# Kernel optimization log

Hardware: AMD Instinct MI355X
Metric: run time of the kernel (lower is better)

## Reference

```python
import jax, jax.numpy as jnp
import numpy as np

SM_SCALE = 0.08838834764831845  # 1/sqrt(128)
Q_LEN, K_LEN, H, M, D = 1024, 1024, 8, 8, 128


def setup_inputs() -> dict:
    key = jax.random.key(0)
    k1, k2, k3, k4 = jax.random.split(key, 4)
    Q = jax.random.normal(k1, (Q_LEN, H, M, D), dtype=jnp.float32)
    K_expanded = jax.random.normal(k2, (K_LEN, H, M, D), dtype=jnp.float32)
    mask = jax.random.normal(k3, (Q_LEN, K_LEN), dtype=jnp.float32)
    sinks = jax.random.normal(k4, (H, M, Q_LEN, 1), dtype=jnp.float32)
    return {"Q": Q, "K_expanded": K_expanded, "mask": mask, "sinks": sinks}


def reference(Q, K_expanded, mask, sinks):
    # [h, m, q, k] scaled scores + additive mask
    QK = jnp.einsum('qhmd,khmd->hmqk', Q, K_expanded) * SM_SCALE
    QK = QK + mask[None, None, :, :]
    # append sink logits on the key axis -> [h, m, q, k+1]
    return jnp.concatenate([QK, sinks], axis=-1)
```

## Files before the change

kernel.cpp:

```cpp
#include <hip/hip_runtime.h>
#include <hip/hip_bf16.h>

#define QL 1024
#define KL 1024
#define HM 64
#define DD 128
#define SM_SCALE 0.08838834764831845f

#define BM 128
#define BN 128
#define LDPAD 136

typedef __bf16 bf16x8 __attribute__((ext_vector_type(8)));
typedef __bf16 bf16x4 __attribute__((ext_vector_type(4)));
typedef float floatx4 __attribute__((ext_vector_type(4)));

__global__ __launch_bounds__(256, 2)
void qk_kernel(const float* __restrict__ Qg, const float* __restrict__ Kg,
               const float* __restrict__ mask, float* __restrict__ out)
{
    const int g    = blockIdx.y;
    const int tile = blockIdx.x;
    const int qt = (tile >> 3) * BM;
    const int kt = (tile & 7) * BN;

    __shared__ __bf16 As[BM][LDPAD];
    __shared__ __bf16 Bs[BN][LDPAD];

    const int t = threadIdx.x;

    const float* Ag = Qg + (size_t)qt * (HM * DD) + (size_t)g * DD;
    const float* Bg = Kg + (size_t)kt * (HM * DD) + (size_t)g * DD;
#pragma unroll
    for (int j = 0; j < 16; ++j) {
        int c = t + 256 * j;
        int row = c >> 5;
        int c4  = c & 31;
        float4 a = *(const float4*)(Ag + (size_t)row * (HM * DD) + c4 * 4);
        float4 b = *(const float4*)(Bg + (size_t)row * (HM * DD) + c4 * 4);
        bf16x4 av = { (__bf16)a.x, (__bf16)a.y, (__bf16)a.z, (__bf16)a.w };
        bf16x4 bv = { (__bf16)b.x, (__bf16)b.y, (__bf16)b.z, (__bf16)b.w };
        *(bf16x4*)&As[row][c4 * 4] = av;
        *(bf16x4*)&Bs[row][c4 * 4] = bv;
    }
    __syncthreads();

    const int wave = t >> 6;
    const int lane = t & 63;
    const int wm = (wave & 1) * 64;
    const int wn = (wave >> 1) * 64;
    const int lr = lane & 15;
    const int quad = lane >> 4;

    floatx4 acc[4][4] = {};

#pragma unroll
    for (int ks = 0; ks < 4; ++ks) {
        const int d0 = ks * 32 + quad * 8;
        bf16x8 af[4], bf[4];
#pragma unroll
        for (int mi = 0; mi < 4; ++mi)
            af[mi] = *(const bf16x8*)&As[wm + mi * 16 + lr][d0];
#pragma unroll
        for (int ni = 0; ni < 4; ++ni)
            bf[ni] = *(const bf16x8*)&Bs[wn + ni * 16 + lr][d0];
#pragma unroll
        for (int mi = 0; mi < 4; ++mi)
#pragma unroll
            for (int ni = 0; ni < 4; ++ni)
                acc[mi][ni] = __builtin_amdgcn_mfma_f32_16x16x32_bf16(
                    af[mi], bf[ni], acc[mi][ni], 0, 0, 0);
    }

    const size_t obase = (size_t)g * QL * 1025;
#pragma unroll
    for (int mi = 0; mi < 4; ++mi) {
#pragma unroll
        for (int r = 0; r < 4; ++r) {
            int q = qt + wm + mi * 16 + quad * 4 + r;
            const float* mrow = mask + (size_t)q * KL;
            float* orow = out + obase + (size_t)q * 1025;
#pragma unroll
            for (int ni = 0; ni < 4; ++ni) {
                int k = kt + wn + ni * 16 + lr;
                orow[k] = acc[mi][ni][r] * SM_SCALE + mrow[k];
            }
        }
    }
}

__global__ void sink_kernel(const float* __restrict__ sinks, float* __restrict__ out)
{
    int idx = blockIdx.x * 256 + threadIdx.x;
    out[(size_t)idx * 1025 + 1024] = sinks[idx];
}

extern "C" void kernel_launch(void* const* d_in, const int* in_sizes, int n_in,
                              void* d_out, int out_size, void* d_ws, size_t ws_size,
                              hipStream_t stream)
{
    const float* Q     = (const float*)d_in[0];
    const float* K     = (const float*)d_in[1];
    const float* mask  = (const float*)d_in[2];
    const float* sinks = (const float*)d_in[3];
    float* out = (float*)d_out;

    sink_kernel<<<(HM * QL) / 256, 256, 0, stream>>>(sinks, out);
    qk_kernel<<<dim3(64, 64), 256, 0, stream>>>(Q, K, mask, out);
}
```

Baseline: 410.3 us.

## Pre-convert Q/K to bf16 workspace and stream K tiles with async LDS loads

Adds a conversion kernel that writes Q and K as head-contiguous bf16 into the workspace. The original kernel re-read fp32 Q and K for every 128x128 tile. A new main kernel keeps one Q tile's fragments in registers and loops over all 8 K tiles per block. Each K tile is fetched with global_load_lds async copies into an XOR-swizzled LDS buffer, overlapping the next tile's fetch with the current MFMA and output stores. Sink writes are folded into the same kernel, which adds an extra launch and workspace traffic but cuts redundant fp32 reads. The grid shrinks to 512 blocks, which may reduce occupancy on a large GPU.

```diff
diff --git a/kernel.cpp b/kernel.cpp
--- a/kernel.cpp
+++ b/kernel.cpp
@@ -7,13 +7,147 @@
 #define DD 128
 #define SM_SCALE 0.08838834764831845f
 
+typedef __bf16 bf16x8_t __attribute__((ext_vector_type(8)));
+typedef __bf16 bf16x4_t __attribute__((ext_vector_type(4)));
+typedef float floatx4_t __attribute__((ext_vector_type(4)));
+
+__device__ __forceinline__ void async_cp16(const void* g, void* l) {
+    __builtin_amdgcn_global_load_lds(
+        (const __attribute__((address_space(1))) void*)g,
+        (__attribute__((address_space(3))) void*)l, 16, 0, 0);
+}
+
+__global__ __launch_bounds__(256)
+void cvt_kernel(const float* __restrict__ Q, const float* __restrict__ K,
+                __bf16* __restrict__ Qb, __bf16* __restrict__ Kb)
+{
+    const int g = blockIdx.y, rc = blockIdx.x, t = threadIdx.x;
+    const size_t inb  = (size_t)(rc * 128) * (HM * DD) + (size_t)g * DD;
+    const size_t outb = (size_t)g * (QL * DD) + (size_t)(rc * 128) * DD;
+#pragma unroll
+    for (int j = 0; j < 16; ++j) {
+        int c = t + 256 * j, row = c >> 5, c4 = c & 31;
+        size_t go = inb + (size_t)row * (HM * DD) + c4 * 4;
+        size_t wo = outb + (size_t)row * DD + c4 * 4;
+        float4 a = *(const float4*)(Q + go);
+        float4 b = *(const float4*)(K + go);
+        bf16x4_t av = { (__bf16)a.x, (__bf16)a.y, (__bf16)a.z, (__bf16)a.w };
+        bf16x4_t bv = { (__bf16)b.x, (__bf16)b.y, (__bf16)b.z, (__bf16)b.w };
+        *(bf16x4_t*)(Qb + wo) = av;
+        *(bf16x4_t*)(Kb + wo) = bv;
+    }
+}
+
+__global__ __launch_bounds__(256, 2)
+void qk2_kernel(const __bf16* __restrict__ Qb, const __bf16* __restrict__ Kb,
+                const float* __restrict__ mask, const float* __restrict__ sinks,
+                float* __restrict__ out)
+{
+    const int g  = blockIdx.y;
+    const int qt = blockIdx.x * 128;
+
+    __shared__ __bf16 As[128 * DD];
+    __shared__ __bf16 Bs[128 * DD];
+
+    const int t = threadIdx.x, wave = t >> 6, lane = t & 63;
+    const int lr = lane & 15, quad = lane >> 4;
+    const int wm = (wave & 1) * 64, wn = (wave >> 1) * 64;
+
+    const __bf16* Atile  = Qb + (size_t)g * QL * DD + (size_t)qt * DD;
+    const __bf16* Ktile0 = Kb + (size_t)g * KL * DD;
+
+#pragma unroll
+    for (int i = 0; i < 8; ++i) {
+        int r = wave * 32 + i * 4 + (lane >> 4);
+        int s = lane & 15;
+        int c = s ^ (r & 15);
+        async_cp16(Atile + (size_t)r * DD + c * 8, As + (wave * 32 + i * 4) * DD);
+    }
+#pragma unroll
+    for (int i = 0; i < 8; ++i) {
+        int r = wave * 32 + i * 4 + (lane >> 4);
+        int s = lane & 15;
+        int c = s ^ (r & 15);
+        async_cp16(Ktile0 + (size_t)r * DD + c * 8, Bs + (wave * 32 + i * 4) * DD);
+    }
+    asm volatile("s_waitcnt vmcnt(0)" ::: "memory");
+    __syncthreads();
+
+    bf16x8_t af[4][4];
+#pragma unroll
+    for (int ks = 0; ks < 4; ++ks)
+#pragma unroll
+        for (int mi = 0; mi < 4; ++mi) {
+            int r = wm + mi * 16 + lr;
+            int c = ks * 4 + quad;
+            af[ks][mi] = *(const bf16x8_t*)&As[r * DD + (c ^ lr) * 8];
+        }
+
+    const size_t outg = (size_t)g * QL * 1025;
+
+#pragma unroll 1
+    for (int kt = 0; kt < 8; ++kt) {
+        bf16x8_t bfr[4][4];
+#pragma unroll
+        for (int ks = 0; ks < 4; ++ks)
+#pragma unroll
+            for (int ni = 0; ni < 4; ++ni) {
+                int r = wn + ni * 16 + lr;
+                int c = ks * 4 + quad;
+                bfr[ks][ni] = *(const bf16x8_t*)&Bs[r * DD + (c ^ lr) * 8];
+            }
+        __syncthreads();
+
+        if (kt < 7) {
+            const __bf16* Kt = Ktile0 + (size_t)(kt + 1) * 128 * DD;
+#pragma unroll
+            for (int i = 0; i < 8; ++i) {
+                int r = wave * 32 + i * 4 + (lane >> 4);
+                int s = lane & 15;
+                int c = s ^ (r & 15);
+                async_cp16(Kt + (size_t)r * DD + c * 8, Bs + (wave * 32 + i * 4) * DD);
+            }
+        }
+
+        floatx4_t acc[4][4] = {};
+#pragma unroll
+        for (int ks = 0; ks < 4; ++ks)
+#pragma unroll
+            for (int mi = 0; mi < 4; ++mi)
+#pragma unroll
+                for (int ni = 0; ni < 4; ++ni)
+                    acc[mi][ni] = __builtin_amdgcn_mfma_f32_16x16x32_bf16(
+                        af[ks][mi], bfr[ks][ni], acc[mi][ni], 0, 0, 0);
+
+#pragma unroll
+        for (int mi = 0; mi < 4; ++mi)
+#pragma unroll
+            for (int r4 = 0; r4 < 4; ++r4) {
+                int q = qt + wm + mi * 16 + quad * 4 + r4;
+                const float* mrow = mask + (size_t)q * KL + kt * 128;
+                float* orow = out + outg + (size_t)q * 1025 + kt * 128;
+#pragma unroll
+                for (int ni = 0; ni < 4; ++ni) {
+                    int k = wn + ni * 16 + lr;
+                    orow[k] = acc[mi][ni][r4] * SM_SCALE + mrow[k];
+                }
+            }
+
+        if (kt < 7) {
+            asm volatile("s_waitcnt vmcnt(0)" ::: "memory");
+            __syncthreads();
+        }
+    }
+
+    if (t < 128) {
+        int q = qt + t;
+        out[outg + (size_t)q * 1025 + 1024] = sinks[(size_t)g * QL + q];
+    }
+}
+
 #define BM 128
 #define BN 128
 #define LDPAD 136
-
-typedef __bf16 bf16x8 __attribute__((ext_vector_type(8)));
-typedef __bf16 bf16x4 __attribute__((ext_vector_type(4)));
-typedef float floatx4 __attribute__((ext_vector_type(4)));
 
 __global__ __launch_bounds__(256, 2)
 void qk_kernel(const float* __restrict__ Qg, const float* __restrict__ Kg,
@@ -38,10 +172,10 @@
         int c4  = c & 31;
         float4 a = *(const float4*)(Ag + (size_t)row * (HM * DD) + c4 * 4);
         float4 b = *(const float4*)(Bg + (size_t)row * (HM * DD) + c4 * 4);
-        bf16x4 av = { (__bf16)a.x, (__bf16)a.y, (__bf16)a.z, (__bf16)a.w };
-        bf16x4 bv = { (__bf16)b.x, (__bf16)b.y, (__bf16)b.z, (__bf16)b.w };
-        *(bf16x4*)&As[row][c4 * 4] = av;
-        *(bf16x4*)&Bs[row][c4 * 4] = bv;
+        bf16x4_t av = { (__bf16)a.x, (__bf16)a.y, (__bf16)a.z, (__bf16)a.w };
+        bf16x4_t bv = { (__bf16)b.x, (__bf16)b.y, (__bf16)b.z, (__bf16)b.w };
+        *(bf16x4_t*)&As[row][c4 * 4] = av;
+        *(bf16x4_t*)&Bs[row][c4 * 4] = bv;
     }
     __syncthreads();
 
@@ -52,24 +186,24 @@
     const int lr = lane & 15;
     const int quad = lane >> 4;
 
-    floatx4 acc[4][4] = {};
+    floatx4_t acc[4][4] = {};
 
 #pragma unroll
     for (int ks = 0; ks < 4; ++ks) {
         const int d0 = ks * 32 + quad * 8;
-        bf16x8 af[4], bf[4];
+        bf16x8_t a8[4], b8[4];
 #pragma unroll
         for (int mi = 0; mi < 4; ++mi)
-            af[mi] = *(const bf16x8*)&As[wm + mi * 16 + lr][d0];
+            a8[mi] = *(const bf16x8_t*)&As[wm + mi * 16 + lr][d0];
 #pragma unroll
         for (int ni = 0; ni < 4; ++ni)
-            bf[ni] = *(const bf16x8*)&Bs[wn + ni * 16 + lr][d0];
+            b8[ni] = *(const bf16x8_t*)&Bs[wn + ni * 16 + lr][d0];
 #pragma unroll
         for (int mi = 0; mi < 4; ++mi)
 #pragma unroll
             for (int ni = 0; ni < 4; ++ni)
                 acc[mi][ni] = __builtin_amdgcn_mfma_f32_16x16x32_bf16(
-                    af[mi], bf[ni], acc[mi][ni], 0, 0, 0);
+                    a8[mi], b8[ni], acc[mi][ni], 0, 0, 0);
     }
 
     const size_t obase = (size_t)g * QL * 1025;
@@ -105,6 +239,14 @@
     const float* sinks = (const float*)d_in[3];
     float* out = (float*)d_out;
 
-    sink_kernel<<<(HM * QL) / 256, 256, 0, stream>>>(sinks, out);
-    qk_kernel<<<dim3(64, 64), 256, 0, stream>>>(Q, K, mask, out);
-}
+    const size_t need = (size_t)2 * QL * HM * DD * sizeof(__bf16);
+    if (ws_size >= need) {
+        __bf16* Qb = (__bf16*)d_ws;
+        __bf16* Kb = Qb + (size_t)QL * HM * DD;
+        cvt_kernel<<<dim3(8, 64), 256, 0, stream>>>(Q, K, Qb, Kb);
+        qk2_kernel<<<dim3(8, 64), 256, 0, stream>>>(Qb, Kb, mask, sinks, out);
+    } else {
+        sink_kernel<<<(HM * QL) / 256, 256, 0, stream>>>(sinks, out);
+        qk_kernel<<<dim3(64, 64), 256, 0, stream>>>(Q, K, mask, out);
+    }
+}
```

Measured after the change: 425.7 us. 3.7% more time.
